# Performance work log

Measured on AMD Instinct MI355X. Metric: run time of the kernel, lower is better.

## Reference

```python
import jax, jax.numpy as jnp
import numpy as np

N_NODES = 100000
N_EDGES = 1600000
C_IN = 64
C_OUT = 64
BN_EPS = 1e-5


def setup_inputs() -> dict:
    key = jax.random.key(0)
    k_x, k_e, k_w, k_b, k_g = jax.random.split(key, 5)
    x = jax.random.normal(k_x, (N_NODES, C_IN), dtype=jnp.float32)
    edge_index = jax.random.randint(k_e, (2, N_EDGES), 0, N_NODES, dtype=jnp.int64)
    # Linear(in_channels*2, out_channels)
    lim = 1.0 / np.sqrt(2 * C_IN)
    W = jax.random.uniform(k_w, (2 * C_IN, C_OUT), dtype=jnp.float32, minval=-lim, maxval=lim)
    b = jax.random.uniform(k_b, (C_OUT,), dtype=jnp.float32, minval=-lim, maxval=lim)
    # BatchNorm affine params
    gamma = jnp.ones((C_OUT,), dtype=jnp.float32)
    beta = jnp.zeros((C_OUT,), dtype=jnp.float32)
    return {"x": x, "edge_index": edge_index, "W": W, "b": b, "gamma": gamma, "beta": beta}


def reference(x, edge_index, W, b, gamma, beta):
    src = edge_index[0]  # j (source)
    dst = edge_index[1]  # i (target)
    x_i = x[dst]                      # [E, C_IN]
    x_j = x[src]                      # [E, C_IN]
    # EdgeConv message: mlp(concat(x_i, x_j - x_i))
    feat = jnp.concatenate([x_i, x_j - x_i], axis=-1)  # [E, 2*C_IN]
    msg = feat @ W + b                                  # [E, C_OUT]
    # max aggregation back to target nodes; empty nodes -> 0 (PyG convention)
    agg = jax.ops.segment_max(msg, dst, num_segments=N_NODES)
    agg = jnp.where(jnp.isneginf(agg), 0.0, agg)
    h = jax.nn.elu(agg)
    # BatchNorm1d over nodes (training-mode batch stats, biased variance)
    mean = jnp.mean(h, axis=0)
    var = jnp.var(h, axis=0)
    return gamma * (h - mean) / jnp.sqrt(var + BN_EPS) + beta
```

## Files before the change

### kernel.cpp

```cpp
#include <hip/hip_runtime.h>
#include <math.h>

#define N_NODES 100000
#define N_EDGES 1600000
#define C 64
#define BKT_SHIFT 6
#define BKT_NODES 64
#define NBKT 1563
#define BKT_CAP 2048
#define TILE 8192
#define BIN_THREADS 1024
#define MAXW 65
#define NSTRIPE 32
#define XSTR 72
#define BN_EPS 1e-5f

typedef __attribute__((ext_vector_type(8))) short short8;
typedef __attribute__((ext_vector_type(4))) float f32x4;


__device__ __forceinline__ float eluf(float x) {
    return x > 0.f ? x : (expf(x) - 1.f);
}

__device__ __forceinline__ float key32_to_f(unsigned k32) {
    unsigned k16 = k32 >> 16;
    unsigned u16 = (k16 & 0x8000u) ? (k16 & 0x7FFFu) : (~k16 & 0xFFFFu);
    return __uint_as_float(u16 << 16);
}
__device__ __forceinline__ unsigned bf16rne(float f) {
    unsigned u = __float_as_uint(f);
    return (u + 0x7FFFu + ((u >> 16) & 1u)) >> 16;
}
__device__ __forceinline__ float bf16lo_f(unsigned w) { return __uint_as_float((w & 0xFFFFu) << 16); }
__device__ __forceinline__ float bf16hi_f(unsigned w) { return __uint_as_float(w & 0xFFFF0000u); }

__global__ __launch_bounds__(256) void k_init(unsigned* __restrict__ bcnt,
                                              float* __restrict__ stripes) {
    int t = blockIdx.x * blockDim.x + threadIdx.x;
    if (t < NBKT) bcnt[t] = 0u;
    if (t < NSTRIPE * 128) stripes[t] = 0.f;
}

__global__ __launch_bounds__(BIN_THREADS) void k_bin(const int* __restrict__ ei,
                                                     unsigned* __restrict__ bcnt,
                                                     unsigned* __restrict__ binned) {
    __shared__ unsigned hcnt[NBKT];
    __shared__ unsigned hbase[NBKT];
    int e0 = blockIdx.x * TILE;
    int ecount = min(TILE, N_EDGES - e0);
    if (ecount <= 0) return;

    for (int i = threadIdx.x; i < NBKT; i += BIN_THREADS) hcnt[i] = 0u;
    __syncthreads();
    for (int i = threadIdx.x; i < ecount; i += BIN_THREADS) {
        int dst = ei[N_EDGES + e0 + i];
        if ((unsigned)dst < N_NODES) atomicAdd(&hcnt[dst >> BKT_SHIFT], 1u);
    }
    __syncthreads();
    for (int i = threadIdx.x; i < NBKT; i += BIN_THREADS) {
        unsigned c = hcnt[i];
        hbase[i] = c ? atomicAdd(&bcnt[i], c) : 0u;
        hcnt[i] = 0u;
    }
    __syncthreads();
    for (int i = threadIdx.x; i < ecount; i += BIN_THREADS) {
        int src = ei[e0 + i];
        int dst = ei[N_EDGES + e0 + i];
        if ((unsigned)src >= N_NODES || (unsigned)dst >= N_NODES) continue;
        int bk = dst >> BKT_SHIFT;
        unsigned pos = hbase[bk] + atomicAdd(&hcnt[bk], 1u);
        if (pos < BKT_CAP)
            binned[(size_t)bk * BKT_CAP + pos] =
                ((unsigned)(dst & (BKT_NODES - 1)) << 17) | (unsigned)src;
    }
}

__global__ __launch_bounds__(256) void k_gemm(const float* __restrict__ x,
                                              const float* __restrict__ W,
                                              const float* __restrict__ b,
                                              unsigned* __restrict__ Apb,
                                              unsigned* __restrict__ Bkey) {
    __shared__ unsigned short WaT[64 * XSTR];
    __shared__ unsigned short WbT[64 * XSTR];
    __shared__ unsigned short xB[128 * XSTR];
    __shared__ float biasS[64];
    int t = threadIdx.x;
    int base = blockIdx.x * 128;

    for (int p = t; p < 4096; p += 256) {
        int k = p >> 6, c = p & 63;
        float w1 = W[p];
        float w2 = W[4096 + p];
        WaT[c * XSTR + k] = (unsigned short)bf16rne(w1 - w2);
        WbT[c * XSTR + k] = (unsigned short)bf16rne(w2);
    }
    if (t < 64) biasS[t] = b[t];

    {
        int node = t >> 1;
        int c0 = (t & 1) * 32;
        int gnode = base + node;
        float v[32];
        if (gnode < N_NODES) {
            const float4* xp = (const float4*)(x + (size_t)gnode * 64 + c0);
#pragma unroll
            for (int i = 0; i < 8; ++i) {
                float4 f = xp[i];
                v[4 * i + 0] = f.x; v[4 * i + 1] = f.y;
                v[4 * i + 2] = f.z; v[4 * i + 3] = f.w;
            }
        } else {
#pragma unroll
            for (int i = 0; i < 32; ++i) v[i] = 0.f;
        }
        unsigned short* dst = &xB[node * XSTR + c0];
#pragma unroll
        for (int i = 0; i < 32; ++i) dst[i] = (unsigned short)bf16rne(v[i]);
    }
    __syncthreads();

    int w = t >> 6;
    int l = t & 63;
    int ln = l & 15;
    int hi = l >> 4;

    short8 wa[4][2], wb[4][2];
#pragma unroll
    for (int nt = 0; nt < 4; ++nt)
#pragma unroll
        for (int h = 0; h < 2; ++h) {
            wa[nt][h] = *(const short8*)&WaT[(nt * 16 + ln) * XSTR + h * 32 + hi * 8];
            wb[nt][h] = *(const short8*)&WbT[(nt * 16 + ln) * XSTR + h * 32 + hi * 8];
        }

#pragma unroll
    for (int ph = 0; ph < 2; ++ph) {
        int rowbase = ph * 64 + w * 16;
        short8 af[2];
#pragma unroll
        for (int h = 0; h < 2; ++h)
            af[h] = *(const short8*)&xB[(rowbase + ln) * XSTR + h * 32 + hi * 8];

        f32x4 acca[4], accb[4];
#pragma unroll
        for (int nt = 0; nt < 4; ++nt) {
            acca[nt] = (f32x4){0.f, 0.f, 0.f, 0.f};
            accb[nt] = (f32x4){0.f, 0.f, 0.f, 0.f};
#pragma unroll
            for (int h = 0; h < 2; ++h) {
                acca[nt] = __builtin_amdgcn_mfma_f32_16x16x32_bf16(af[h], wa[nt][h], acca[nt], 0, 0, 0);
                accb[nt] = __builtin_amdgcn_mfma_f32_16x16x32_bf16(af[h], wb[nt][h], accb[nt], 0, 0, 0);
            }
        }
#pragma unroll
        for (int nt = 0; nt < 4; ++nt) {
            int col = nt * 16 + ln;
            float bias = biasS[col];
            int cp = nt * 8 + (ln >> 1);
#pragma unroll
            for (int r = 0; r < 4; ++r) {
                int node = base + rowbase + hi * 4 + r;
                unsigned a16 = bf16rne(acca[nt][r] + bias);
                unsigned aO = (unsigned)__shfl_xor((int)a16, 1, 64);
                unsigned r16 = bf16rne(accb[nt][r]);
                unsigned key16 = (r16 & 0x8000u) ? (~r16 & 0xFFFFu) : (r16 | 0x8000u);
                unsigned kO = (unsigned)__shfl_xor((int)key16, 1, 64);
                if (((l & 1) == 0) && node < N_NODES) {
                    Apb[(size_t)node * 32 + cp] = a16 | (aO << 16);
                    Bkey[(size_t)node * 32 + cp] = key16 | (kO << 16);
                }
            }
        }
    }
}

__global__ __launch_bounds__(256) void k_fused(const unsigned* __restrict__ bcnt,
                                               const unsigned* __restrict__ binned,
                                               const unsigned* __restrict__ Bkey,
                                               const unsigned* __restrict__ Apb,
                                               unsigned* __restrict__ hpk,
                                               float* __restrict__ stripes) {
    extern __shared__ unsigned mx[];
    int q = blockIdx.x;
    int t = threadIdx.x;
    int n0 = q * BKT_NODES;
    int nspan = min(BKT_NODES, N_NODES - n0);

    for (int i = t; i < BKT_NODES * MAXW; i += 256) mx[i] = 0u;
    __syncthreads();

    unsigned cnt = min(bcnt[q], (unsigned)BKT_CAP);
    const unsigned* lst = binned + (size_t)q * BKT_CAP;
    int ls = t & 3;
    for (unsigned i = (unsigned)(t >> 2); i < cnt; i += 64) {
        unsigned p = lst[i];
        unsigned src = p & 0x1FFFFu;
        unsigned dl = p >> 17;
        const uint4* bk = (const uint4*)(Bkey + (size_t)src * 32);
        uint4 w0 = bk[ls];
        uint4 w1 = bk[4 + ls];
        unsigned* row = mx + dl * MAXW;
        int s0 = ls * 8;
        atomicMax(&row[s0 + 0], w0.x << 16);
        atomicMax(&row[s0 + 1], w0.x & 0xFFFF0000u);
        atomicMax(&row[s0 + 2], w0.y << 16);
        atomicMax(&row[s0 + 3], w0.y & 0xFFFF0000u);
        atomicMax(&row[s0 + 4], w0.z << 16);
        atomicMax(&row[s0 + 5], w0.z & 0xFFFF0000u);
        atomicMax(&row[s0 + 6], w0.w << 16);
        atomicMax(&row[s0 + 7], w0.w & 0xFFFF0000u);
        int s1 = 32 + ls * 8;
        atomicMax(&row[s1 + 0], w1.x << 16);
        atomicMax(&row[s1 + 1], w1.x & 0xFFFF0000u);
        atomicMax(&row[s1 + 2], w1.y << 16);
        atomicMax(&row[s1 + 3], w1.y & 0xFFFF0000u);
        atomicMax(&row[s1 + 4], w1.z << 16);
        atomicMax(&row[s1 + 5], w1.z & 0xFFFF0000u);
        atomicMax(&row[s1 + 6], w1.w << 16);
        atomicMax(&row[s1 + 7], w1.w & 0xFFFF0000u);
    }
    __syncthreads();

    int lane4 = t & 15;
    int g = t >> 4;
    float4 s = make_float4(0.f, 0.f, 0.f, 0.f);
    float4 sq = make_float4(0.f, 0.f, 0.f, 0.f);
    for (int nl = g; nl < nspan; nl += 16) {
        int n = n0 + nl;
        const unsigned* row = mx + nl * MAXW + lane4 * 4;
        unsigned k0 = row[0], k1 = row[1], k2 = row[2], k3 = row[3];
        uint2 ap = *reinterpret_cast<const uint2*>(Apb + (size_t)n * 32 + lane4 * 2);
        float h0 = (k0 == 0u) ? 0.f : eluf(bf16lo_f(ap.x) + key32_to_f(k0));
        float h1 = (k1 == 0u) ? 0.f : eluf(bf16hi_f(ap.x) + key32_to_f(k1));
        float h2 = (k2 == 0u) ? 0.f : eluf(bf16lo_f(ap.y) + key32_to_f(k2));
        float h3 = (k3 == 0u) ? 0.f : eluf(bf16hi_f(ap.y) + key32_to_f(k3));
        unsigned q0 = bf16rne(h0), q1 = bf16rne(h1), q2 = bf16rne(h2), q3 = bf16rne(h3);
        uint2 hp;
        hp.x = q0 | (q1 << 16);
        hp.y = q2 | (q3 << 16);
        *reinterpret_cast<uint2*>(hpk + (size_t)n * 32 + lane4 * 2) = hp;
        float f0 = __uint_as_float(q0 << 16), f1 = __uint_as_float(q1 << 16);
        float f2 = __uint_as_float(q2 << 16), f3 = __uint_as_float(q3 << 16);
        s.x += f0; s.y += f1; s.z += f2; s.w += f3;
        sq.x += f0 * f0; sq.y += f1 * f1; sq.z += f2 * f2; sq.w += f3 * f3;
    }
    __syncthreads();

    float4* lsum = (float4*)mx;
    float4* lqum = lsum + 256;
    lsum[t] = s;
    lqum[t] = sq;
    __syncthreads();
#pragma unroll
    for (int off = 8; off >= 1; off >>= 1) {
        if (g < off) {
            int o = t + off * 16;
            lsum[t].x += lsum[o].x; lsum[t].y += lsum[o].y; lsum[t].z += lsum[o].z; lsum[t].w += lsum[o].w;
            lqum[t].x += lqum[o].x; lqum[t].y += lqum[o].y; lqum[t].z += lqum[o].z; lqum[t].w += lqum[o].w;
        }
        __syncthreads();
    }
    if (g == 0) {
        float* sb = stripes + (q & (NSTRIPE - 1)) * 128;
        int c4 = lane4 * 4;
        atomicAdd(&sb[c4 + 0], lsum[t].x);
        atomicAdd(&sb[c4 + 1], lsum[t].y);
        atomicAdd(&sb[c4 + 2], lsum[t].z);
        atomicAdd(&sb[c4 + 3], lsum[t].w);
        atomicAdd(&sb[64 + c4 + 0], lqum[t].x);
        atomicAdd(&sb[64 + c4 + 1], lqum[t].y);
        atomicAdd(&sb[64 + c4 + 2], lqum[t].z);
        atomicAdd(&sb[64 + c4 + 3], lqum[t].w);
    }
}

__global__ __launch_bounds__(128) void k_reduce(const float* __restrict__ stripes,
                                                float* __restrict__ finals) {
    int t = threadIdx.x;
    float acc = 0.f;
#pragma unroll
    for (int s = 0; s < NSTRIPE; ++s) acc += stripes[s * 128 + t];
    finals[t] = acc;
}

__global__ __launch_bounds__(256) void k_bn(const uint2* __restrict__ hpk2,
                                            const float* __restrict__ finals,
                                            const float* __restrict__ gamma,
                                            const float* __restrict__ beta,
                                            float4* __restrict__ out4) {
    size_t i = (size_t)blockIdx.x * blockDim.x + threadIdx.x;
    size_t stride = (size_t)gridDim.x * blockDim.x;
    const float invN = 1.f / (float)N_NODES;
    size_t total4 = (size_t)N_NODES * C / 4;
    for (size_t p = i; p < total4; p += stride) {
        int c4 = (int)(p & 15) * 4;
        uint2 hp = hpk2[p];
        float hx = bf16lo_f(hp.x), hy = bf16hi_f(hp.x);
        float hz = bf16lo_f(hp.y), hw = bf16hi_f(hp.y);
        float4 o;
        float m, v, inv;
        m = finals[c4 + 0] * invN; v = finals[64 + c4 + 0] * invN - m * m; inv = rsqrtf(v + BN_EPS);
        o.x = gamma[c4 + 0] * (hx - m) * inv + beta[c4 + 0];
        m = finals[c4 + 1] * invN; v = finals[64 + c4 + 1] * invN - m * m; inv = rsqrtf(v + BN_EPS);
        o.y = gamma[c4 + 1] * (hy - m) * inv + beta[c4 + 1];
        m = finals[c4 + 2] * invN; v = finals[64 + c4 + 2] * invN - m * m; inv = rsqrtf(v + BN_EPS);
        o.z = gamma[c4 + 2] * (hz - m) * inv + beta[c4 + 2];
        m = finals[c4 + 3] * invN; v = finals[64 + c4 + 3] * invN - m * m; inv = rsqrtf(v + BN_EPS);
        o.w = gamma[c4 + 3] * (hw - m) * inv + beta[c4 + 3];
        out4[p] = o;
    }
}

extern "C" void kernel_launch(void* const* d_in, const int* in_sizes, int n_in,
                              void* d_out, int out_size, void* d_ws, size_t ws_size,
                              hipStream_t stream) {
    const float* x = (const float*)d_in[0];
    const int* ei = (const int*)d_in[1];
    const float* W = (const float*)d_in[2];
    const float* b = (const float*)d_in[3];
    const float* gamma = (const float*)d_in[4];
    const float* beta = (const float*)d_in[5];
    float* out = (float*)d_out;

    char* ws = (char*)d_ws;
    unsigned* Bkey = (unsigned*)ws;
    unsigned* binned = (unsigned*)(ws + (size_t)N_NODES * 32 * 4);
    unsigned* Apb = (unsigned*)((char*)binned + (size_t)NBKT * BKT_CAP * 4);
    unsigned* hpk = Apb + (size_t)N_NODES * 32;
    unsigned* bcnt = hpk + (size_t)N_NODES * 32;
    float* stripes = (float*)((char*)bcnt + ((NBKT * 4 + 255) & ~255));
    float* finals = stripes + NSTRIPE * 128;

    k_init<<<(NSTRIPE * 128 + NBKT + 255) / 256, 256, 0, stream>>>(bcnt, stripes);
    k_bin<<<(N_EDGES + TILE - 1) / TILE, BIN_THREADS, 0, stream>>>(ei, bcnt, binned);
    k_gemm<<<(N_NODES + 127) / 128, 256, 0, stream>>>(x, W, b, Apb, Bkey);
    k_fused<<<NBKT, 256, BKT_NODES * MAXW * 4, stream>>>(bcnt, binned, Bkey, Apb, hpk, stripes);
    k_reduce<<<1, 128, 0, stream>>>(stripes, finals);
    k_bn<<<2048, 256, 0, stream>>>((const uint2*)hpk, finals, gamma, beta, (float4*)out);
}
```

Baseline: 92.68 us.

## Merge edge binning and node GEMM into one heterogeneous prep kernel

The separate binning and GEMM kernels become a single launch. The first block range bins edges by destination bucket, and the remaining blocks compute the per-node bf16 MFMA projections. The GEMM blocks now use 1024 threads covering 256 nodes each, and they load x rows directly from global memory into MFMA fragments instead of staging them through LDS. This removes one kernel launch and lets the two independent stages run concurrently on the GPU. The cost is one block size for both roles and reloading W per larger block. The fused kernel's shared memory switches from dynamic to static sizing.

```diff
diff --git a/kernel.cpp b/kernel.cpp
--- a/kernel.cpp
+++ b/kernel.cpp
@@ -9,7 +9,8 @@
 #define NBKT 1563
 #define BKT_CAP 2048
 #define TILE 8192
-#define BIN_THREADS 1024
+#define NBINB 196
+#define NGEMB 391
 #define MAXW 65
 #define NSTRIPE 32
 #define XSTR 72
@@ -22,7 +23,6 @@
 __device__ __forceinline__ float eluf(float x) {
     return x > 0.f ? x : (expf(x) - 1.f);
 }
-
 __device__ __forceinline__ float key32_to_f(unsigned k32) {
     unsigned k16 = k32 >> 16;
     unsigned u16 = (k16 & 0x8000u) ? (k16 & 0x7FFFu) : (~k16 & 0xFFFFu);
@@ -34,6 +34,15 @@
 }
 __device__ __forceinline__ float bf16lo_f(unsigned w) { return __uint_as_float((w & 0xFFFFu) << 16); }
 __device__ __forceinline__ float bf16hi_f(unsigned w) { return __uint_as_float(w & 0xFFFF0000u); }
+
+__device__ __forceinline__ short8 pack8(float4 a, float4 b) {
+    short8 r;
+    r[0] = (short)bf16rne(a.x); r[1] = (short)bf16rne(a.y);
+    r[2] = (short)bf16rne(a.z); r[3] = (short)bf16rne(a.w);
+    r[4] = (short)bf16rne(b.x); r[5] = (short)bf16rne(b.y);
+    r[6] = (short)bf16rne(b.z); r[7] = (short)bf16rne(b.w);
+    return r;
+}
 
 __global__ __launch_bounds__(256) void k_init(unsigned* __restrict__ bcnt,
                                               float* __restrict__ stripes) {
@@ -42,105 +51,89 @@
     if (t < NSTRIPE * 128) stripes[t] = 0.f;
 }
 
-__global__ __launch_bounds__(BIN_THREADS) void k_bin(const int* __restrict__ ei,
-                                                     unsigned* __restrict__ bcnt,
-                                                     unsigned* __restrict__ binned) {
-    __shared__ unsigned hcnt[NBKT];
-    __shared__ unsigned hbase[NBKT];
-    int e0 = blockIdx.x * TILE;
-    int ecount = min(TILE, N_EDGES - e0);
-    if (ecount <= 0) return;
-
-    for (int i = threadIdx.x; i < NBKT; i += BIN_THREADS) hcnt[i] = 0u;
-    __syncthreads();
-    for (int i = threadIdx.x; i < ecount; i += BIN_THREADS) {
-        int dst = ei[N_EDGES + e0 + i];
-        if ((unsigned)dst < N_NODES) atomicAdd(&hcnt[dst >> BKT_SHIFT], 1u);
-    }
-    __syncthreads();
-    for (int i = threadIdx.x; i < NBKT; i += BIN_THREADS) {
-        unsigned c = hcnt[i];
-        hbase[i] = c ? atomicAdd(&bcnt[i], c) : 0u;
-        hcnt[i] = 0u;
-    }
-    __syncthreads();
-    for (int i = threadIdx.x; i < ecount; i += BIN_THREADS) {
-        int src = ei[e0 + i];
-        int dst = ei[N_EDGES + e0 + i];
-        if ((unsigned)src >= N_NODES || (unsigned)dst >= N_NODES) continue;
-        int bk = dst >> BKT_SHIFT;
-        unsigned pos = hbase[bk] + atomicAdd(&hcnt[bk], 1u);
-        if (pos < BKT_CAP)
-            binned[(size_t)bk * BKT_CAP + pos] =
-                ((unsigned)(dst & (BKT_NODES - 1)) << 17) | (unsigned)src;
-    }
-}
-
-__global__ __launch_bounds__(256) void k_gemm(const float* __restrict__ x,
-                                              const float* __restrict__ W,
-                                              const float* __restrict__ b,
-                                              unsigned* __restrict__ Apb,
-                                              unsigned* __restrict__ Bkey) {
-    __shared__ unsigned short WaT[64 * XSTR];
-    __shared__ unsigned short WbT[64 * XSTR];
-    __shared__ unsigned short xB[128 * XSTR];
-    __shared__ float biasS[64];
+__global__ __launch_bounds__(1024) void k_prep(const int* __restrict__ ei,
+                                               const float* __restrict__ x,
+                                               const float* __restrict__ W,
+                                               const float* __restrict__ b,
+                                               unsigned* __restrict__ bcnt,
+                                               unsigned* __restrict__ binned,
+                                               unsigned* __restrict__ Apb,
+                                               unsigned* __restrict__ Bkey) {
+    __shared__ __align__(16) unsigned char smem[18688];
     int t = threadIdx.x;
-    int base = blockIdx.x * 128;
-
-    for (int p = t; p < 4096; p += 256) {
-        int k = p >> 6, c = p & 63;
-        float w1 = W[p];
-        float w2 = W[4096 + p];
-        WaT[c * XSTR + k] = (unsigned short)bf16rne(w1 - w2);
-        WbT[c * XSTR + k] = (unsigned short)bf16rne(w2);
-    }
-    if (t < 64) biasS[t] = b[t];
-
-    {
-        int node = t >> 1;
-        int c0 = (t & 1) * 32;
-        int gnode = base + node;
-        float v[32];
-        if (gnode < N_NODES) {
-            const float4* xp = (const float4*)(x + (size_t)gnode * 64 + c0);
-#pragma unroll
-            for (int i = 0; i < 8; ++i) {
-                float4 f = xp[i];
-                v[4 * i + 0] = f.x; v[4 * i + 1] = f.y;
-                v[4 * i + 2] = f.z; v[4 * i + 3] = f.w;
+
+    if (blockIdx.x < NBINB) {
+        unsigned* hcnt = (unsigned*)smem;
+        unsigned* hbase = hcnt + NBKT;
+        int e0 = blockIdx.x * TILE;
+        int ecount = min(TILE, N_EDGES - e0);
+
+        for (int i = t; i < NBKT; i += 1024) hcnt[i] = 0u;
+        __syncthreads();
+        for (int i = t; i < ecount; i += 1024) {
+            int dst = ei[N_EDGES + e0 + i];
+            if ((unsigned)dst < N_NODES) atomicAdd(&hcnt[dst >> BKT_SHIFT], 1u);
+        }
+        __syncthreads();
+        for (int i = t; i < NBKT; i += 1024) {
+            unsigned c = hcnt[i];
+            hbase[i] = c ? atomicAdd(&bcnt[i], c) : 0u;
+            hcnt[i] = 0u;
+        }
+        __syncthreads();
+        for (int i = t; i < ecount; i += 1024) {
+            int src = ei[e0 + i];
+            int dst = ei[N_EDGES + e0 + i];
+            if ((unsigned)src >= N_NODES || (unsigned)dst >= N_NODES) continue;
+            int bk = dst >> BKT_SHIFT;
+            unsigned pos = hbase[bk] + atomicAdd(&hcnt[bk], 1u);
+            if (pos < BKT_CAP)
+                binned[(size_t)bk * BKT_CAP + pos] =
+                    ((unsigned)(dst & (BKT_NODES - 1)) << 17) | (unsigned)src;
+        }
+    } else {
+        unsigned short* WaT = (unsigned short*)smem;
+        unsigned short* WbT = WaT + 64 * XSTR;
+        float* biasS = (float*)(WbT + 64 * XSTR);
+        int gb = blockIdx.x - NBINB;
+        int base = gb * 256;
+
+        for (int p = t; p < 4096; p += 1024) {
+            int k = p >> 6, c = p & 63;
+            float w1 = W[p];
+            float w2 = W[4096 + p];
+            WaT[c * XSTR + k] = (unsigned short)bf16rne(w1 - w2);
+            WbT[c * XSTR + k] = (unsigned short)bf16rne(w2);
+        }
+        if (t < 64) biasS[t] = b[t];
+        __syncthreads();
+
+        int w = t >> 6;
+        int l = t & 63;
+        int ln = l & 15;
+        int hi = l >> 4;
+
+        short8 wa[4][2], wb[4][2];
+#pragma unroll
+        for (int nt = 0; nt < 4; ++nt)
+#pragma unroll
+            for (int h = 0; h < 2; ++h) {
+                wa[nt][h] = *(const short8*)&WaT[(nt * 16 + ln) * XSTR + h * 32 + hi * 8];
+                wb[nt][h] = *(const short8*)&WbT[(nt * 16 + ln) * XSTR + h * 32 + hi * 8];
             }
+
+        int arow = base + w * 16 + ln;
+        short8 af[2];
+        if (arow < N_NODES) {
+            const float4* xr = (const float4*)(x + (size_t)arow * 64);
+#pragma unroll
+            for (int h = 0; h < 2; ++h)
+                af[h] = pack8(xr[h * 8 + hi * 2], xr[h * 8 + hi * 2 + 1]);
         } else {
 #pragma unroll
-            for (int i = 0; i < 32; ++i) v[i] = 0.f;
-        }
-        unsigned short* dst = &xB[node * XSTR + c0];
-#pragma unroll
-        for (int i = 0; i < 32; ++i) dst[i] = (unsigned short)bf16rne(v[i]);
-    }
-    __syncthreads();
-
-    int w = t >> 6;
-    int l = t & 63;
-    int ln = l & 15;
-    int hi = l >> 4;
-
-    short8 wa[4][2], wb[4][2];
-#pragma unroll
-    for (int nt = 0; nt < 4; ++nt)
-#pragma unroll
-        for (int h = 0; h < 2; ++h) {
-            wa[nt][h] = *(const short8*)&WaT[(nt * 16 + ln) * XSTR + h * 32 + hi * 8];
-            wb[nt][h] = *(const short8*)&WbT[(nt * 16 + ln) * XSTR + h * 32 + hi * 8];
-        }
-
-#pragma unroll
-    for (int ph = 0; ph < 2; ++ph) {
-        int rowbase = ph * 64 + w * 16;
-        short8 af[2];
-#pragma unroll
-        for (int h = 0; h < 2; ++h)
-            af[h] = *(const short8*)&xB[(rowbase + ln) * XSTR + h * 32 + hi * 8];
+            for (int h = 0; h < 2; ++h)
+                af[h] = (short8){0, 0, 0, 0, 0, 0, 0, 0};
+        }
 
         f32x4 acca[4], accb[4];
 #pragma unroll
@@ -160,7 +153,7 @@
             int cp = nt * 8 + (ln >> 1);
 #pragma unroll
             for (int r = 0; r < 4; ++r) {
-                int node = base + rowbase + hi * 4 + r;
+                int node = base + w * 16 + hi * 4 + r;
                 unsigned a16 = bf16rne(acca[nt][r] + bias);
                 unsigned aO = (unsigned)__shfl_xor((int)a16, 1, 64);
                 unsigned r16 = bf16rne(accb[nt][r]);
@@ -181,7 +174,7 @@
                                                const unsigned* __restrict__ Apb,
                                                unsigned* __restrict__ hpk,
                                                float* __restrict__ stripes) {
-    extern __shared__ unsigned mx[];
+    __shared__ __align__(16) unsigned mx[BKT_NODES * MAXW];
     int q = blockIdx.x;
     int t = threadIdx.x;
     int n0 = q * BKT_NODES;
@@ -333,9 +326,8 @@
     float* finals = stripes + NSTRIPE * 128;
 
     k_init<<<(NSTRIPE * 128 + NBKT + 255) / 256, 256, 0, stream>>>(bcnt, stripes);
-    k_bin<<<(N_EDGES + TILE - 1) / TILE, BIN_THREADS, 0, stream>>>(ei, bcnt, binned);
-    k_gemm<<<(N_NODES + 127) / 128, 256, 0, stream>>>(x, W, b, Apb, Bkey);
-    k_fused<<<NBKT, 256, BKT_NODES * MAXW * 4, stream>>>(bcnt, binned, Bkey, Apb, hpk, stripes);
+    k_prep<<<NBINB + NGEMB, 1024, 0, stream>>>(ei, x, W, b, bcnt, binned, Apb, Bkey);
+    k_fused<<<NBKT, 256, 0, stream>>>(bcnt, binned, Bkey, Apb, hpk, stripes);
     k_reduce<<<1, 128, 0, stream>>>(stripes, finals);
     k_bn<<<2048, 256, 0, stream>>>((const uint2*)hpk, finals, gamma, beta, (float4*)out);
 }
```

Result: faster. 86.11 us (-7.1%).
